# Performance work log

Hardware: AMD Instinct MI355X
Metric: run time of the kernel (lower is better)

The kernel has to match this reference:

```python
import jax, jax.numpy as jnp
import numpy as np

EPS = 1e-12  # undefined global `eps` in the original source; standard tiny epsilon


def setup_inputs() -> dict:
    key = jax.random.key(0)
    k1, k2 = jax.random.split(key)
    B, C = 32768, 1000
    output = jax.random.normal(k1, (B, C), dtype=jnp.float32)
    multilabels = (jax.random.uniform(k2, (B, C)) < 0.05).astype(jnp.float32)
    multilabels = multilabels.at[:, 0].set(1.0)
    return {"output": output, "multilabels": multilabels}


def reference(output, multilabels):
    # Equivalent closed form of: for every nonempty subset g of true labels,
    #   loss(g) = -[ pseudo_y*log(o+eps) + (1-pseudo_y)*log(1-o+eps) ].sum()
    #           = base - sum_{j in g} gain_j,
    # with base = -sum_j log(1-o_j+eps) and gain_j = log(o_j+eps)-log(1-o_j+eps).
    # min over nonempty subsets = base - max nonempty-subset gain
    #   = base - (sum of positive gains over true labels, or the max single
    #      gain among true labels if all gains are negative).
    o = jax.nn.sigmoid(output)                      # [B, C]
    log_p = jnp.log(o + EPS)
    log_np = jnp.log(1.0 - o + EPS)
    base = -jnp.sum(log_np, axis=1)                 # [B]
    gain = log_p - log_np                           # [B, C]
    is_true = multilabels == 1.0                    # [B, C] bool (constant)
    pos = is_true & (gain > 0)
    pos_gain = jnp.sum(jnp.where(pos, gain, 0.0), axis=1)          # [B]
    any_pos = jnp.any(pos, axis=1)                                  # [B]
    best_single = jnp.max(jnp.where(is_true, gain, -jnp.inf), axis=1)  # [B]
    max_gain = jnp.where(any_pos, pos_gain, best_single)
    per_sample = base - max_gain                    # [B]
    return jnp.mean(per_sample)
```

## Files before the change

### kernel.cpp

```cpp
#include <hip/hip_runtime.h>
#include <math.h>


constexpr int B = 32768;
constexpr int C = 1000;
constexpr int C4 = C / 4;
constexpr int THREADS = 256;

typedef float f32x4 __attribute__((ext_vector_type(4)));

__device__ __forceinline__ void elem_update(float x, float m,
                                            float& base, float& pos, float& best) {
    float e  = __expf(-fabsf(x));
    float xp = fmaxf(x, 0.0f);
    base += xp + __logf(1.0f + e);
    pos  += m * xp;
    if (m != 0.0f) best = fmaxf(best, x);
}

__global__ __launch_bounds__(THREADS)
void row_loss_kernel(const float* __restrict__ X,
                     const float* __restrict__ M,
                     float* __restrict__ partial) {
    const int row = blockIdx.x;
    const int t   = threadIdx.x;

    float base = 0.f, pos = 0.f, best = -INFINITY;

    if (t < C4) {
        const f32x4* x4 = reinterpret_cast<const f32x4*>(X + (size_t)row * C);
        const f32x4* m4 = reinterpret_cast<const f32x4*>(M + (size_t)row * C);
        f32x4 x = __builtin_nontemporal_load(x4 + t);
        f32x4 m = __builtin_nontemporal_load(m4 + t);
        elem_update(x.x, m.x, base, pos, best);
        elem_update(x.y, m.y, base, pos, best);
        elem_update(x.z, m.z, base, pos, best);
        elem_update(x.w, m.w, base, pos, best);
    }

    #pragma unroll
    for (int off = 32; off > 0; off >>= 1) {
        base += __shfl_down(base, off, 64);
        pos  += __shfl_down(pos,  off, 64);
        best  = fmaxf(best, __shfl_down(best, off, 64));
    }

    __shared__ float sb[4], sp[4], ss[4];
    const int w    = t >> 6;
    const int lane = t & 63;
    if (lane == 0) { sb[w] = base; sp[w] = pos; ss[w] = best; }
    __syncthreads();
    if (t == 0) {
        float b = (sb[0] + sb[1]) + (sb[2] + sb[3]);
        float p = (sp[0] + sp[1]) + (sp[2] + sp[3]);
        float s = fmaxf(fmaxf(ss[0], ss[1]), fmaxf(ss[2], ss[3]));
        partial[row] = b - ((p > 0.f) ? p : s);
    }
}

__global__ __launch_bounds__(256)
void finalize1_kernel(const float* __restrict__ partial, float* __restrict__ mid) {
    const int b = blockIdx.x;
    const int t = threadIdx.x;
    float v = partial[b * 512 + t] + partial[b * 512 + t + 256];

    #pragma unroll
    for (int off = 32; off > 0; off >>= 1)
        v += __shfl_down(v, off, 64);

    __shared__ float s[4];
    const int w    = t >> 6;
    const int lane = t & 63;
    if (lane == 0) s[w] = v;
    __syncthreads();
    if (t == 0) mid[b] = (s[0] + s[1]) + (s[2] + s[3]);
}

__global__ __launch_bounds__(64)
void finalize2_kernel(const float* __restrict__ mid, float* __restrict__ out) {
    double v = (double)mid[threadIdx.x];
    #pragma unroll
    for (int off = 32; off > 0; off >>= 1)
        v += __shfl_down(v, off, 64);
    if (threadIdx.x == 0) out[0] = (float)(v / (double)B);
}

extern "C" void kernel_launch(void* const* d_in, const int* in_sizes, int n_in,
                              void* d_out, int out_size, void* d_ws, size_t ws_size,
                              hipStream_t stream) {
    const float* X  = (const float*)d_in[0];
    const float* M  = (const float*)d_in[1];
    float* out      = (float*)d_out;
    float* partial  = (float*)d_ws;
    float* mid      = partial + B;

    row_loss_kernel<<<B, THREADS, 0, stream>>>(X, M, partial);
    finalize1_kernel<<<64, 256, 0, stream>>>(partial, mid);
    finalize2_kernel<<<1, 64, 0, stream>>>(mid, out);
}
```

Baseline: 245.9 us.

## Map one row per wavefront with multiple vector loads per lane

Each 256-thread block now processes four rows, one per 64-lane wavefront, with each lane issuing four 16-byte loads for X and M. This removes the cross-wave shared-memory reduction and __syncthreads, and raises memory-level parallelism per thread. The tail chunk is padded with values that contribute nothing to the sums. Register use grows somewhat and the grid shrinks by four.

```diff
diff --git a/kernel.cpp b/kernel.cpp
--- a/kernel.cpp
+++ b/kernel.cpp
@@ -4,8 +4,8 @@
 
 constexpr int B = 32768;
 constexpr int C = 1000;
-constexpr int C4 = C / 4;
 constexpr int THREADS = 256;
+constexpr int TAIL = 250 - 192;
 
 typedef float f32x4 __attribute__((ext_vector_type(4)));
 
@@ -18,25 +18,51 @@
     if (m != 0.0f) best = fmaxf(best, x);
 }
 
+__device__ __forceinline__ void vec_update(const f32x4& x, const f32x4& m,
+                                           float& base, float& pos, float& best) {
+    elem_update(x.x, m.x, base, pos, best);
+    elem_update(x.y, m.y, base, pos, best);
+    elem_update(x.z, m.z, base, pos, best);
+    elem_update(x.w, m.w, base, pos, best);
+}
+
 __global__ __launch_bounds__(THREADS)
 void row_loss_kernel(const float* __restrict__ X,
                      const float* __restrict__ M,
                      float* __restrict__ partial) {
-    const int row = blockIdx.x;
-    const int t   = threadIdx.x;
+    const int t    = threadIdx.x;
+    const int w    = t >> 6;
+    const int lane = t & 63;
+    const int row  = blockIdx.x * 4 + w;
 
-    float base = 0.f, pos = 0.f, best = -INFINITY;
+    const f32x4* x4 = reinterpret_cast<const f32x4*>(X + (size_t)row * C);
+    const f32x4* m4 = reinterpret_cast<const f32x4*>(M + (size_t)row * C);
 
-    if (t < C4) {
-        const f32x4* x4 = reinterpret_cast<const f32x4*>(X + (size_t)row * C);
-        const f32x4* m4 = reinterpret_cast<const f32x4*>(M + (size_t)row * C);
-        f32x4 x = __builtin_nontemporal_load(x4 + t);
-        f32x4 m = __builtin_nontemporal_load(m4 + t);
-        elem_update(x.x, m.x, base, pos, best);
-        elem_update(x.y, m.y, base, pos, best);
-        elem_update(x.z, m.z, base, pos, best);
-        elem_update(x.w, m.w, base, pos, best);
+    f32x4 x0 = __builtin_nontemporal_load(x4 + lane);
+    f32x4 x1 = __builtin_nontemporal_load(x4 + lane + 64);
+    f32x4 x2 = __builtin_nontemporal_load(x4 + lane + 128);
+    f32x4 m0 = __builtin_nontemporal_load(m4 + lane);
+    f32x4 m1 = __builtin_nontemporal_load(m4 + lane + 64);
+    f32x4 m2 = __builtin_nontemporal_load(m4 + lane + 128);
+    f32x4 x3 = {-1e30f, -1e30f, -1e30f, -1e30f};
+    f32x4 m3 = {0.f, 0.f, 0.f, 0.f};
+    if (lane < TAIL) {
+        x3 = __builtin_nontemporal_load(x4 + lane + 192);
+        m3 = __builtin_nontemporal_load(m4 + lane + 192);
     }
+
+    float b0 = 0.f, b1 = 0.f, b2 = 0.f, b3 = 0.f;
+    float p0 = 0.f, p1 = 0.f, p2 = 0.f, p3 = 0.f;
+    float s0 = -INFINITY, s1 = -INFINITY, s2 = -INFINITY, s3 = -INFINITY;
+
+    vec_update(x0, m0, b0, p0, s0);
+    vec_update(x1, m1, b1, p1, s1);
+    vec_update(x2, m2, b2, p2, s2);
+    vec_update(x3, m3, b3, p3, s3);
+
+    float base = (b0 + b1) + (b2 + b3);
+    float pos  = (p0 + p1) + (p2 + p3);
+    float best = fmaxf(fmaxf(s0, s1), fmaxf(s2, s3));
 
     #pragma unroll
     for (int off = 32; off > 0; off >>= 1) {
@@ -45,17 +71,8 @@
         best  = fmaxf(best, __shfl_down(best, off, 64));
     }
 
-    __shared__ float sb[4], sp[4], ss[4];
-    const int w    = t >> 6;
-    const int lane = t & 63;
-    if (lane == 0) { sb[w] = base; sp[w] = pos; ss[w] = best; }
-    __syncthreads();
-    if (t == 0) {
-        float b = (sb[0] + sb[1]) + (sb[2] + sb[3]);
-        float p = (sp[0] + sp[1]) + (sp[2] + sp[3]);
-        float s = fmaxf(fmaxf(ss[0], ss[1]), fmaxf(ss[2], ss[3]));
-        partial[row] = b - ((p > 0.f) ? p : s);
-    }
+    if (lane == 0)
+        partial[row] = base - ((pos > 0.f) ? pos : best);
 }
 
 __global__ __launch_bounds__(256)
@@ -94,7 +111,7 @@
     float* partial  = (float*)d_ws;
     float* mid      = partial + B;
 
-    row_loss_kernel<<<B, THREADS, 0, stream>>>(X, M, partial);
+    row_loss_kernel<<<B / 4, THREADS, 0, stream>>>(X, M, partial);
     finalize1_kernel<<<64, 256, 0, stream>>>(partial, mid);
     finalize2_kernel<<<1, 64, 0, stream>>>(mid, out);
 }
```

Measured after the change: 247.8 us. No clear change (+0.8%).
